# Optimization experiments

Hardware: AMD Instinct MI355X
Metric: run time of the kernel (lower is better)

## Reference

```python
import jax, jax.numpy as jnp
import numpy as np

LAMBDA = 5.0  # lambda_ init arg


def setup_inputs() -> dict:
    key = jax.random.key(0)
    k1, k2 = jax.random.split(key)
    B, D, K = 131072, 512, 112
    return {
        "x": jax.random.normal(k1, (B, D), dtype=jnp.float32),
        "cluster_centers": jax.random.normal(k2, (K, D), dtype=jnp.float32),
        "topk": 5,
    }


def reference(x, cluster_centers, topk):
    # similarity to all cluster centers: [B, K]
    sims = x @ cluster_centers.T
    # top-k cluster indices per row: [B, k]
    _, idx = jax.lax.top_k(sims, topk)
    # gather selected centers: [B, k, D]
    Ac = cluster_centers[idx]
    # re-score selected centers against the query, softmax over k
    scores = jax.nn.softmax(jnp.einsum('bkd,bd->bk', Ac, x), axis=-1)
    # softmax-weighted aggregation, scaled, plus residual
    Tc = LAMBDA * jnp.einsum('bk,bkd->bd', scores, Ac)
    return Tc + x
```

## Files before the change

### kernel.cpp

```cpp
#include <hip/hip_runtime.h>
#include <math.h>

#define D_DIM 512
#define K_DIM 112
#define TOPK 5
#define LAMBDA_ 5.0f

#define BM 128
#define BK 64
#define TM 8
#define TN 7
#define NTHREADS 256

struct __align__(16) SMem {
  union {
    struct {
      float xs[BK][BM + 4];
      float cs[BK][K_DIM + 4];
    } g;
    struct {
      float sims[BM][K_DIM + 1];
      float sc[BM][TOPK];
      int   si[BM][TOPK];
    } p;
  } u;
};

__global__ __launch_bounds__(NTHREADS, 2)
void tse_fused(const float* __restrict__ x, const float* __restrict__ cc,
               float* __restrict__ out) {
  __shared__ SMem sm;
  const int tid = threadIdx.x;
  const int tx = tid & 15;
  const int ky = tid >> 4;
  const long long row0 = (long long)blockIdx.x * BM;

  float acc[TM][TN];
#pragma unroll
  for (int i = 0; i < TM; ++i)
#pragma unroll
    for (int j = 0; j < TN; ++j) acc[i][j] = 0.0f;

  for (int dc = 0; dc < D_DIM; dc += BK) {
#pragma unroll
    for (int it = 0; it < (BM * BK / 4) / NTHREADS; ++it) {
      int id = it * NTHREADS + tid;
      int r  = id >> 4;
      int dg = id & 15;
      float4 v = *(const float4*)(x + (row0 + r) * D_DIM + dc + dg * 4);
      sm.u.g.xs[dg * 4 + 0][r] = v.x;
      sm.u.g.xs[dg * 4 + 1][r] = v.y;
      sm.u.g.xs[dg * 4 + 2][r] = v.z;
      sm.u.g.xs[dg * 4 + 3][r] = v.w;
    }
#pragma unroll
    for (int it = 0; it < (K_DIM * BK / 4) / NTHREADS; ++it) {
      int id = it * NTHREADS + tid;
      int k  = id >> 4;
      int dg = id & 15;
      float4 v = *(const float4*)(cc + (long long)k * D_DIM + dc + dg * 4);
      sm.u.g.cs[dg * 4 + 0][k] = v.x;
      sm.u.g.cs[dg * 4 + 1][k] = v.y;
      sm.u.g.cs[dg * 4 + 2][k] = v.z;
      sm.u.g.cs[dg * 4 + 3][k] = v.w;
    }
    __syncthreads();

#pragma unroll 4
    for (int d = 0; d < BK; ++d) {
      float4 xa = *(const float4*)&sm.u.g.xs[d][tx * TM];
      float4 xb = *(const float4*)&sm.u.g.xs[d][tx * TM + 4];
      float xf[TM] = {xa.x, xa.y, xa.z, xa.w, xb.x, xb.y, xb.z, xb.w};
      float cf[TN];
#pragma unroll
      for (int j = 0; j < TN; ++j) cf[j] = sm.u.g.cs[d][ky * TN + j];
#pragma unroll
      for (int i = 0; i < TM; ++i)
#pragma unroll
        for (int j = 0; j < TN; ++j)
          acc[i][j] = fmaf(xf[i], cf[j], acc[i][j]);
    }
    __syncthreads();
  }

#pragma unroll
  for (int i = 0; i < TM; ++i)
#pragma unroll
    for (int j = 0; j < TN; ++j)
      sm.u.p.sims[tx * TM + i][ky * TN + j] = acc[i][j];
  __syncthreads();

  if (tid < BM) {
    float tv[TOPK];
    int   ti[TOPK];
#pragma unroll
    for (int i = 0; i < TOPK; ++i) { tv[i] = -3.0e38f; ti[i] = 0; }
    for (int k = 0; k < K_DIM; ++k) {
      float v = sm.u.p.sims[tid][k];
      if (v > tv[TOPK - 1]) {
        tv[TOPK - 1] = v; ti[TOPK - 1] = k;
#pragma unroll
        for (int i = TOPK - 2; i >= 0; --i) {
          if (tv[i + 1] > tv[i]) {
            float tf = tv[i]; tv[i] = tv[i + 1]; tv[i + 1] = tf;
            int   tq = ti[i]; ti[i] = ti[i + 1]; ti[i + 1] = tq;
          }
        }
      }
    }
    float m = tv[0];
    float e[TOPK];
    float z = 0.0f;
#pragma unroll
    for (int i = 0; i < TOPK; ++i) { e[i] = __expf(tv[i] - m); z += e[i]; }
    float s = LAMBDA_ / z;
#pragma unroll
    for (int i = 0; i < TOPK; ++i) {
      sm.u.p.sc[tid][i] = e[i] * s;
      sm.u.p.si[tid][i] = ti[i];
    }
  }
  __syncthreads();

  {
    const int dg = tid & 127;
    int r = tid >> 7;
    for (; r < BM; r += NTHREADS / 128) {
      const long long base = (row0 + r) * D_DIM + dg * 4;
      float4 o = *(const float4*)(x + base);
#pragma unroll
      for (int t = 0; t < TOPK; ++t) {
        float w  = sm.u.p.sc[r][t];
        int   ix = sm.u.p.si[r][t];
        float4 cv = *(const float4*)(cc + (long long)ix * D_DIM + dg * 4);
        o.x = fmaf(w, cv.x, o.x);
        o.y = fmaf(w, cv.y, o.y);
        o.z = fmaf(w, cv.z, o.z);
        o.w = fmaf(w, cv.w, o.w);
      }
      *(float4*)(out + base) = o;
    }
  }
}

extern "C" void kernel_launch(void* const* d_in, const int* in_sizes, int n_in,
                              void* d_out, int out_size, void* d_ws, size_t ws_size,
                              hipStream_t stream) {
  const float* x  = (const float*)d_in[0];
  const float* cc = (const float*)d_in[1];
  float* out = (float*)d_out;
  const int Btot = in_sizes[0] / D_DIM;
  const int grid = Btot / BM;
  tse_fused<<<dim3(grid), dim3(NTHREADS), 0, stream>>>(x, cc, out);
}
```

Baseline: 690.1 us.

## Pre-transpose centers to global, read from L1/L2, and do two-stage per-thread top-k

Adds a small pre-kernel that transposes the cluster centers into a padded global buffer. The main GEMM then reads centers straight from global/cache instead of staging them in shared memory, and only the x tile goes through LDS, now with an XOR swizzle. The block shrinks to 128 threads, each computing an 8x14 tile. Top-k becomes two stages: each thread picks per-row candidates from its own 14 columns in registers, then one thread per row merges 40 candidates, which replaces the full similarity matrix in shared memory. The risks are higher register pressure, fewer threads per block, and an extra kernel launch.

```diff
diff --git a/kernel.cpp b/kernel.cpp
--- a/kernel.cpp
+++ b/kernel.cpp
@@ -3,25 +3,37 @@
 
 #define D_DIM 512
 #define K_DIM 112
-#define TOPK 5
+#define TOPK  5
 #define LAMBDA_ 5.0f
 
 #define BM 128
 #define BK 64
 #define TM 8
-#define TN 7
-#define NTHREADS 256
+#define TN 14
+#define NTHREADS 128
+#define XS_LD 132
+#define CT_LD 128
+#define NCAND (8 * TOPK)
+#define CAND_LD 41
+
+__device__ float g_ct[D_DIM * CT_LD];
+
+__global__ __launch_bounds__(128)
+void transpose_c(const float* __restrict__ cc) {
+  const int d = blockIdx.x;
+  const int k = threadIdx.x;
+  if (k < K_DIM)
+    g_ct[d * CT_LD + (k / TN) * 16 + (k % TN)] = cc[k * D_DIM + d];
+}
 
 struct __align__(16) SMem {
   union {
+    float xs[BK * XS_LD];
     struct {
-      float xs[BK][BM + 4];
-      float cs[BK][K_DIM + 4];
-    } g;
-    struct {
-      float sims[BM][K_DIM + 1];
-      float sc[BM][TOPK];
-      int   si[BM][TOPK];
+      float         cv[BM][CAND_LD];
+      unsigned char ci[BM][CAND_LD];
+      float         sc[BM][TOPK];
+      int           si[BM][TOPK];
     } p;
   } u;
 };
@@ -31,8 +43,8 @@
                float* __restrict__ out) {
   __shared__ SMem sm;
   const int tid = threadIdx.x;
-  const int tx = tid & 15;
-  const int ky = tid >> 4;
+  const int ky  = tid & 7;
+  const int tx  = tid >> 3;
   const long long row0 = (long long)blockIdx.x * BM;
 
   float acc[TM][TN];
@@ -41,39 +53,36 @@
 #pragma unroll
     for (int j = 0; j < TN; ++j) acc[i][j] = 0.0f;
 
+#pragma unroll 1
   for (int dc = 0; dc < D_DIM; dc += BK) {
 #pragma unroll
     for (int it = 0; it < (BM * BK / 4) / NTHREADS; ++it) {
-      int id = it * NTHREADS + tid;
-      int r  = id >> 4;
-      int dg = id & 15;
+      int t  = it * NTHREADS + tid;
+      int dg = t & 15;
+      int r  = t >> 4;
       float4 v = *(const float4*)(x + (row0 + r) * D_DIM + dc + dg * 4);
-      sm.u.g.xs[dg * 4 + 0][r] = v.x;
-      sm.u.g.xs[dg * 4 + 1][r] = v.y;
-      sm.u.g.xs[dg * 4 + 2][r] = v.z;
-      sm.u.g.xs[dg * 4 + 3][r] = v.w;
-    }
-#pragma unroll
-    for (int it = 0; it < (K_DIM * BK / 4) / NTHREADS; ++it) {
-      int id = it * NTHREADS + tid;
-      int k  = id >> 4;
-      int dg = id & 15;
-      float4 v = *(const float4*)(cc + (long long)k * D_DIM + dc + dg * 4);
-      sm.u.g.cs[dg * 4 + 0][k] = v.x;
-      sm.u.g.cs[dg * 4 + 1][k] = v.y;
-      sm.u.g.cs[dg * 4 + 2][k] = v.z;
-      sm.u.g.cs[dg * 4 + 3][k] = v.w;
+      int d0 = dg * 4;
+      int rw = r ^ (((dg >> 1) & 7) << 2);
+      sm.u.xs[(d0 + 0) * XS_LD + rw] = v.x;
+      sm.u.xs[(d0 + 1) * XS_LD + rw] = v.y;
+      sm.u.xs[(d0 + 2) * XS_LD + rw] = v.z;
+      sm.u.xs[(d0 + 3) * XS_LD + rw] = v.w;
     }
     __syncthreads();
 
+    const float* ctp = g_ct + dc * CT_LD + ky * 16;
 #pragma unroll 4
-    for (int d = 0; d < BK; ++d) {
-      float4 xa = *(const float4*)&sm.u.g.xs[d][tx * TM];
-      float4 xb = *(const float4*)&sm.u.g.xs[d][tx * TM + 4];
+    for (int dl = 0; dl < BK; ++dl) {
+      const int rho = ((dl >> 3) & 7) << 2;
+      const float* xrow = &sm.u.xs[dl * XS_LD];
+      const int off = (tx * TM) ^ rho;
+      float4 xa = *(const float4*)(xrow + off);
+      float4 xb = *(const float4*)(xrow + (off ^ 4));
       float xf[TM] = {xa.x, xa.y, xa.z, xa.w, xb.x, xb.y, xb.z, xb.w};
-      float cf[TN];
-#pragma unroll
-      for (int j = 0; j < TN; ++j) cf[j] = sm.u.g.cs[d][ky * TN + j];
+      const float4* cp = (const float4*)(ctp + dl * CT_LD);
+      float4 c0 = cp[0], c1 = cp[1], c2 = cp[2], c3 = cp[3];
+      float cf[TN] = {c0.x, c0.y, c0.z, c0.w, c1.x, c1.y, c1.z, c1.w,
+                      c2.x, c2.y, c2.z, c2.w, c3.x, c3.y};
 #pragma unroll
       for (int i = 0; i < TM; ++i)
 #pragma unroll
@@ -84,55 +93,71 @@
   }
 
 #pragma unroll
-  for (int i = 0; i < TM; ++i)
+  for (int i = 0; i < TM; ++i) {
+    float tv[TOPK]; int ti[TOPK];
 #pragma unroll
-    for (int j = 0; j < TN; ++j)
-      sm.u.p.sims[tx * TM + i][ky * TN + j] = acc[i][j];
+    for (int s = 0; s < TOPK; ++s) { tv[s] = -3.0e38f; ti[s] = 0; }
+#pragma unroll
+    for (int j = 0; j < TN; ++j) {
+      float v = acc[i][j];
+      if (v > tv[TOPK - 1]) {
+        tv[TOPK - 1] = v; ti[TOPK - 1] = ky * TN + j;
+#pragma unroll
+        for (int s = TOPK - 2; s >= 0; --s) {
+          if (tv[s + 1] > tv[s]) {
+            float tf = tv[s]; tv[s] = tv[s + 1]; tv[s + 1] = tf;
+            int   tq = ti[s]; ti[s] = ti[s + 1]; ti[s + 1] = tq;
+          }
+        }
+      }
+    }
+    int r = tx * TM + i;
+#pragma unroll
+    for (int s = 0; s < TOPK; ++s) {
+      sm.u.p.cv[r][ky * TOPK + s] = tv[s];
+      sm.u.p.ci[r][ky * TOPK + s] = (unsigned char)ti[s];
+    }
+  }
   __syncthreads();
 
-  if (tid < BM) {
-    float tv[TOPK];
-    int   ti[TOPK];
+  {
+    const int r = tid;
+    float tv[TOPK]; int ti[TOPK];
 #pragma unroll
-    for (int i = 0; i < TOPK; ++i) { tv[i] = -3.0e38f; ti[i] = 0; }
-    for (int k = 0; k < K_DIM; ++k) {
-      float v = sm.u.p.sims[tid][k];
+    for (int s = 0; s < TOPK; ++s) { tv[s] = -3.0e38f; ti[s] = 0; }
+    for (int c = 0; c < NCAND; ++c) {
+      float v = sm.u.p.cv[r][c];
       if (v > tv[TOPK - 1]) {
-        tv[TOPK - 1] = v; ti[TOPK - 1] = k;
+        tv[TOPK - 1] = v; ti[TOPK - 1] = (int)sm.u.p.ci[r][c];
 #pragma unroll
-        for (int i = TOPK - 2; i >= 0; --i) {
-          if (tv[i + 1] > tv[i]) {
-            float tf = tv[i]; tv[i] = tv[i + 1]; tv[i + 1] = tf;
-            int   tq = ti[i]; ti[i] = ti[i + 1]; ti[i + 1] = tq;
+        for (int s = TOPK - 2; s >= 0; --s) {
+          if (tv[s + 1] > tv[s]) {
+            float tf = tv[s]; tv[s] = tv[s + 1]; tv[s + 1] = tf;
+            int   tq = ti[s]; ti[s] = ti[s + 1]; ti[s + 1] = tq;
           }
         }
       }
     }
     float m = tv[0];
-    float e[TOPK];
-    float z = 0.0f;
+    float e[TOPK]; float z = 0.0f;
 #pragma unroll
-    for (int i = 0; i < TOPK; ++i) { e[i] = __expf(tv[i] - m); z += e[i]; }
-    float s = LAMBDA_ / z;
+    for (int s = 0; s < TOPK; ++s) { e[s] = __expf(tv[s] - m); z += e[s]; }
+    float sl = LAMBDA_ / z;
 #pragma unroll
-    for (int i = 0; i < TOPK; ++i) {
-      sm.u.p.sc[tid][i] = e[i] * s;
-      sm.u.p.si[tid][i] = ti[i];
-    }
+    for (int s = 0; s < TOPK; ++s) { sm.u.p.sc[r][s] = e[s] * sl; sm.u.p.si[r][s] = ti[s]; }
   }
   __syncthreads();
 
   {
-    const int dg = tid & 127;
-    int r = tid >> 7;
-    for (; r < BM; r += NTHREADS / 128) {
+    const int dg = tid;
+    for (int r = 0; r < BM; ++r) {
       const long long base = (row0 + r) * D_DIM + dg * 4;
       float4 o = *(const float4*)(x + base);
 #pragma unroll
       for (int t = 0; t < TOPK; ++t) {
         float w  = sm.u.p.sc[r][t];
         int   ix = sm.u.p.si[r][t];
-        float4 cv = *(const float4*)(cc + (long long)ix * D_DIM + dg * 4);
+        const float4 cv = *(const float4*)(cc + (long long)ix * D_DIM + dg * 4);
         o.x = fmaf(w, cv.x, o.x);
         o.y = fmaf(w, cv.y, o.y);
         o.z = fmaf(w, cv.z, o.z);
@@ -151,5 +176,6 @@
   float* out = (float*)d_out;
   const int Btot = in_sizes[0] / D_DIM;
   const int grid = Btot / BM;
+  transpose_c<<<dim3(D_DIM), dim3(128), 0, stream>>>(cc);
   tse_fused<<<dim3(grid), dim3(NTHREADS), 0, stream>>>(x, cc, out);
 }
```

Measured after the change: 807.1 us. +17.0%, slower.
